# Kernel optimization log

Measured on AMD Instinct MI355X. Metric: run time of the kernel, lower is better.

The kernel has to match this reference:

```python
import jax, jax.numpy as jnp
import numpy as np

D = 512
CELLS = 16
BATCH = 4
SEQ = 1024


def setup_inputs() -> dict:
    key = jax.random.key(0)
    ks = jax.random.split(key, 5)
    x = jax.random.normal(ks[0], (BATCH * CELLS, SEQ, D), dtype=jnp.float32)
    # causal mask: True where attention is disallowed (strict upper triangle)
    m = ~jnp.tril(jnp.ones((SEQ, SEQ), dtype=bool))
    gamma = jnp.ones((D,), dtype=jnp.float32)
    beta = jnp.zeros((D,), dtype=jnp.float32)
    Wg = jax.random.normal(ks[1], (D, D), dtype=jnp.float32) * (D ** -0.5)
    inhibit = jax.random.normal(ks[2], (CELLS, CELLS), dtype=jnp.float32) * 0.02
    phases = jnp.linspace(0.0, 2.0 * np.pi, CELLS, dtype=jnp.float32)
    res_scale = jnp.ones((1,), dtype=jnp.float32) * 0.1
    return {"x": x, "m": m, "gamma": gamma, "beta": beta, "Wg": Wg,
            "inhibit": inhibit, "phases": phases, "res_scale": res_scale,
            "B": BATCH, "T": SEQ}


def _layernorm(x, gamma, beta, eps=1e-5):
    mu = jnp.mean(x, axis=-1, keepdims=True)
    var = jnp.var(x, axis=-1, keepdims=True)
    return (x - mu) * jax.lax.rsqrt(var + eps) * gamma + beta


def reference(x, m, gamma, beta, Wg, inhibit, phases, res_scale, B, T):
    d = x.shape[-1]
    cells = inhibit.shape[0]
    nx = _layernorm(x, gamma, beta)
    qkv = nx @ Wg.T                                  # [BC, T, d]
    att = jnp.einsum('bqd,bkd->bqk', qkv, qkv) * (d ** -0.5)  # [BC, T, T]
    att = jnp.where(m, -jnp.inf, att)
    x = x + jax.nn.softmax(att, axis=-1) @ qkv       # [BC, T, d]
    sync = x.reshape(B, cells, T, d)
    competed = jnp.einsum('bctd,ck->bktd', sync, inhibit)
    pulse = jnp.sin(competed + phases[None, :, None, None])
    return x + pulse.reshape(B * cells, T, d) * res_scale
```

## Files before the change

kernel.cpp:

```cpp
#include <hip/hip_runtime.h>
#include <stdint.h>

#define TSEQ 1024
#define DDIM 512

typedef __attribute__((ext_vector_type(8))) short bf16x8;
typedef __attribute__((ext_vector_type(4))) float f32x4;

#define MFMA(a, b, c) __builtin_amdgcn_mfma_f32_16x16x32_bf16((a), (b), (c), 0, 0, 0)

__device__ __forceinline__ unsigned short f2bf(float f) {
  unsigned int u = __builtin_bit_cast(unsigned int, f);
  u += 0x7FFFu + ((u >> 16) & 1u);
  return (unsigned short)(u >> 16);
}

__device__ __forceinline__ void async_load16(const void* g, void* l) {
  __builtin_amdgcn_global_load_lds(
      (const __attribute__((address_space(1))) unsigned int*)g,
      (__attribute__((address_space(3))) unsigned int*)l, 16, 0, 0);
}

__global__ __launch_bounds__(256) void k_ln(const float* __restrict__ x,
                                            const float* __restrict__ gamma,
                                            const float* __restrict__ beta,
                                            unsigned short* __restrict__ nx) {
  const int wid = threadIdx.x >> 6, lane = threadIdx.x & 63;
  const long long row = (long long)blockIdx.x * 4 + wid;
  const float* xr = x + row * DDIM + lane * 8;
  float4 a = *(const float4*)xr;
  float4 b = *(const float4*)(xr + 4);
  float s = a.x + a.y + a.z + a.w + b.x + b.y + b.z + b.w;
  float s2 = a.x * a.x + a.y * a.y + a.z * a.z + a.w * a.w +
             b.x * b.x + b.y * b.y + b.z * b.z + b.w * b.w;
#pragma unroll
  for (int m = 1; m < 64; m <<= 1) {
    s += __shfl_xor(s, m);
    s2 += __shfl_xor(s2, m);
  }
  const float mu = s * (1.0f / DDIM);
  const float var = s2 * (1.0f / DDIM) - mu * mu;
  const float rsd = rsqrtf(var + 1e-5f);
  const float4 g0 = *(const float4*)(gamma + lane * 8);
  const float4 g1 = *(const float4*)(gamma + lane * 8 + 4);
  const float4 b0 = *(const float4*)(beta + lane * 8);
  const float4 b1 = *(const float4*)(beta + lane * 8 + 4);
  float o0 = (a.x - mu) * rsd * g0.x + b0.x;
  float o1 = (a.y - mu) * rsd * g0.y + b0.y;
  float o2 = (a.z - mu) * rsd * g0.z + b0.z;
  float o3 = (a.w - mu) * rsd * g0.w + b0.w;
  float o4 = (b.x - mu) * rsd * g1.x + b1.x;
  float o5 = (b.y - mu) * rsd * g1.y + b1.y;
  float o6 = (b.z - mu) * rsd * g1.z + b1.z;
  float o7 = (b.w - mu) * rsd * g1.w + b1.w;
  uint4 pk;
  pk.x = f2bf(o0) | ((unsigned)f2bf(o1) << 16);
  pk.y = f2bf(o2) | ((unsigned)f2bf(o3) << 16);
  pk.z = f2bf(o4) | ((unsigned)f2bf(o5) << 16);
  pk.w = f2bf(o6) | ((unsigned)f2bf(o7) << 16);
  *(uint4*)(nx + row * DDIM + lane * 8) = pk;
}

__global__ __launch_bounds__(256) void k_cast(const float* __restrict__ w,
                                              unsigned short* __restrict__ o, int n8) {
  const int i = blockIdx.x * 256 + threadIdx.x;
  if (i >= n8) return;
  const float4 a = *(const float4*)(w + (size_t)i * 8);
  const float4 b = *(const float4*)(w + (size_t)i * 8 + 4);
  uint4 pk;
  pk.x = f2bf(a.x) | ((unsigned)f2bf(a.y) << 16);
  pk.y = f2bf(a.z) | ((unsigned)f2bf(a.w) << 16);
  pk.z = f2bf(b.x) | ((unsigned)f2bf(b.y) << 16);
  pk.w = f2bf(b.z) | ((unsigned)f2bf(b.w) << 16);
  *(uint4*)(o + (size_t)i * 8) = pk;
}

__global__ __launch_bounds__(256, 2) void k_gemm(const unsigned short* __restrict__ A,
                                                 const unsigned short* __restrict__ B,
                                                 unsigned short* __restrict__ C) {
  __shared__ char As[16384];
  __shared__ char Bs[16384];
  const int tid = threadIdx.x;
  const int wid = tid >> 6, lane = tid & 63;
  const int g = lane >> 4, c = lane & 15;
  const int wr = wid >> 1, wc = wid & 1;
  const int bm = blockIdx.y, bn = blockIdx.x;

  int srcoff[4], ldsoff[4];
#pragma unroll
  for (int r = 0; r < 4; ++r) {
    const int aoff = r * 4096 + tid * 16;
    srcoff[r] = (aoff >> 7) * 1024 + (aoff & 127);
    ldsoff[r] = r * 4096 + (wid << 10);
  }
  const char* Ab = (const char*)A + (size_t)bm * 131072;
  const char* Bb = (const char*)B + (size_t)bn * 131072;

  f32x4 acc[4][4] = {};

  for (int ks = 0; ks < 8; ++ks) {
    __syncthreads();
#pragma unroll
    for (int r = 0; r < 4; ++r) {
      async_load16(Ab + ks * 128 + srcoff[r], As + ldsoff[r]);
      async_load16(Bb + ks * 128 + srcoff[r], Bs + ldsoff[r]);
    }
    __syncthreads();
    bf16x8 af[4][2], bfr[4][2];
#pragma unroll
    for (int f = 0; f < 4; ++f) {
#pragma unroll
      for (int kk = 0; kk < 2; ++kk) {
        const int rowa = wr * 64 + f * 16 + c;
        af[f][kk] = *(const bf16x8*)(As + rowa * 128 + (kk * 4 + g) * 16);
        const int rowb = wc * 64 + f * 16 + c;
        bfr[f][kk] = *(const bf16x8*)(Bs + rowb * 128 + (kk * 4 + g) * 16);
      }
    }
#pragma unroll
    for (int i = 0; i < 4; ++i) {
#pragma unroll
      for (int j = 0; j < 4; ++j) {
        acc[i][j] = MFMA(af[i][0], bfr[j][0], acc[i][j]);
        acc[i][j] = MFMA(af[i][1], bfr[j][1], acc[i][j]);
      }
    }
  }
#pragma unroll
  for (int i = 0; i < 4; ++i) {
#pragma unroll
    for (int r = 0; r < 4; ++r) {
      const long long row = (long long)bm * 128 + wr * 64 + i * 16 + g * 4 + r;
#pragma unroll
      for (int j = 0; j < 4; ++j) {
        const int col = bn * 128 + wc * 64 + j * 16 + c;
        C[row * DDIM + col] = f2bf(acc[i][j][r]);
      }
    }
  }
}

__global__ __launch_bounds__(256) void k_vt(const unsigned short* __restrict__ qkv,
                                            unsigned short* __restrict__ qkvT) {
  __shared__ unsigned short t[64][72];
  const int ti = blockIdx.x;
  const int di = blockIdx.y;
  const int bc = blockIdx.z;
  const int tid = threadIdx.x;
  const int r = tid >> 3, c8 = tid & 7;
  const unsigned short* src = qkv + ((size_t)bc * TSEQ + ti * 64) * DDIM + di * 64;
#pragma unroll
  for (int p = 0; p < 2; ++p) {
    const bf16x8 v = *(const bf16x8*)(src + (size_t)(r + p * 32) * DDIM + c8 * 8);
    *(bf16x8*)&t[r + p * 32][c8 * 8] = v;
  }
  __syncthreads();
  unsigned short* dst = qkvT + ((size_t)bc * DDIM + di * 64) * TSEQ + ti * 64;
#pragma unroll
  for (int p = 0; p < 2; ++p) {
    const int d = r + p * 32;
    bf16x8 v;
#pragma unroll
    for (int j = 0; j < 8; ++j) v[j] = t[c8 * 8 + j][d];
    *(bf16x8*)(dst + (size_t)d * TSEQ + c8 * 8) = v;
  }
}

__global__ __launch_bounds__(512, 2) void k_attn(const unsigned short* __restrict__ qkv,
                                                 const unsigned short* __restrict__ qkvT,
                                                 const float* __restrict__ x,
                                                 float* __restrict__ xo) {
  __shared__ char lds[131072];
  const int tid = threadIdx.x;
  const int wid = tid >> 6, lane = tid & 63;
  const int g = lane >> 4, c = lane & 15;
  const int bc = blockIdx.x;
  const size_t bcbase = (size_t)bc * TSEQ * DDIM;
  const float scale = 0.044194173824159216f;

  int e0[2], e1[2];
#pragma unroll
  for (int ft = 0; ft < 2; ++ft) {
    const int row = ((c >> 2) << 3) + (ft << 2) + (c & 3);
    const int kap = ((ft << 2) | (c & 3)) ^ ((c >> 2) << 1);
    e0[ft] = row * 1024 + ((g ^ kap) << 4);
    e1[ft] = row * 1024 + (((4 + g) ^ kap) << 4);
  }

  int soffK[4], soffV[4];
#pragma unroll
  for (int r = 0; r < 4; ++r) {
    const int row = wid * 4 + r;
    const int kap = (row & 7) ^ (((row >> 3) & 3) << 1);
    soffK[r] = row * 1024 + ((lane ^ kap) << 4);
    soffV[r] = (wid * 64 + r * 16 + (lane >> 2)) * 2048 + (lane & 3) * 16;
  }
  const char* kgb = (const char*)(qkv + bcbase);
  const char* vgb = (const char*)qkvT + ((size_t)bc << 20);

#pragma unroll 1
  for (int h = 0; h < 2; ++h) {
    const int qt = h == 0 ? 7 - blockIdx.y : blockIdx.y;
    const int qrow = qt * 128 + wid * 16 + c;
    const int NT = 4 * qt + 4;

    bf16x8 qf[16];
    const unsigned short* qp = qkv + bcbase + (size_t)qrow * DDIM + g * 8;
#pragma unroll
    for (int ks = 0; ks < 16; ++ks) qf[ks] = *(const bf16x8*)(qp + ks * 32);

    f32x4 oacc[32] = {};
    float mrun = -1e30f, lrun = 0.0f;

    {
      char* kb = lds;
      char* vb = lds + 65536;
#pragma unroll
      for (int r = 0; r < 4; ++r) {
        async_load16(kgb + soffK[r], kb + wid * 4096 + r * 1024 + lane * 16);
        async_load16(vgb + soffV[r], vb + wid * 4096 + r * 1024 + lane * 16);
      }
    }

    for (int kvt = 0; kvt < NT; ++kvt) {
      __syncthreads();
      const char* kb = lds + (kvt & 1) * 32768;
      const char* vb = lds + 65536 + (kvt & 1) * 32768;

      if (kvt + 1 < NT) {
        char* kd = lds + ((kvt + 1) & 1) * 32768;
        char* vd = lds + 65536 + ((kvt + 1) & 1) * 32768;
        const char* ksrc = kgb + (kvt + 1) * 32768;
        const char* vsrc = vgb + (kvt + 1) * 64;
#pragma unroll
        for (int r = 0; r < 4; ++r) {
          async_load16(ksrc + soffK[r], kd + wid * 4096 + r * 1024 + lane * 16);
          async_load16(vsrc + soffV[r], vd + wid * 4096 + r * 1024 + lane * 16);
        }
      }

      f32x4 st[2] = {};
      __builtin_amdgcn_s_setprio(1);
#pragma unroll
      for (int ks = 0; ks < 16; ++ks) {
        const int imm = (ks >> 1) * 128;
#pragma unroll
        for (int ft = 0; ft < 2; ++ft) {
          const bf16x8 kf = *(const bf16x8*)(kb + imm + ((ks & 1) ? e1[ft] : e0[ft]));
          st[ft] = MFMA(kf, qf[ks], st[ft]);
        }
      }
      __builtin_amdgcn_s_setprio(0);

      float ex[2][4];
      float mt = -1e30f;
#pragma unroll
      for (int ft = 0; ft < 2; ++ft) {
#pragma unroll
        for (int r = 0; r < 4; ++r) {
          const int kvg = kvt * 32 + g * 8 + ft * 4 + r;
          const float v = st[ft][r] * scale;
          ex[ft][r] = (kvg > qrow) ? -1e30f : v;
          mt = fmaxf(mt, ex[ft][r]);
        }
      }
      mt = fmaxf(mt, __shfl_xor(mt, 16));
      mt = fmaxf(mt, __shfl_xor(mt, 32));
      const float mprev = mrun;
      const float mnew = fmaxf(mprev, mt);
      mrun = mnew;
      float psum = 0.0f;
#pragma unroll
      for (int ft = 0; ft < 2; ++ft) {
#pragma unroll
        for (int r = 0; r < 4; ++r) {
          ex[ft][r] = __expf(ex[ft][r] - mnew);
          psum += ex[ft][r];
        }
      }
      psum += __shfl_xor(psum, 16);
      psum += __shfl_xor(psum, 32);

      if (!__all(mt <= mprev)) {
        const float corr = __expf(mprev - mnew);
        lrun = lrun * corr + psum;
        float cr[4];
#pragma unroll
        for (int r = 0; r < 4; ++r) cr[r] = __shfl(corr, g * 4 + r);
#pragma unroll
        for (int dt = 0; dt < 32; ++dt) {
          oacc[dt][0] *= cr[0];
          oacc[dt][1] *= cr[1];
          oacc[dt][2] *= cr[2];
          oacc[dt][3] *= cr[3];
        }
      } else {
        lrun += psum;
      }

      bf16x8 pa0;
#pragma unroll
      for (int r = 0; r < 4; ++r) {
        pa0[r] = (short)f2bf(ex[0][r]);
        pa0[r + 4] = (short)f2bf(ex[1][r]);
      }

      const char* vp = vb + c * 64 + g * 16;
#pragma unroll
      for (int dt = 0; dt < 32; ++dt) {
        const bf16x8 b0 = *(const bf16x8*)(vp + dt * 1024);
        oacc[dt] = MFMA(pa0, b0, oacc[dt]);
      }
    }

    const float rl = 1.0f / lrun;
    float rlr[4];
#pragma unroll
    for (int r = 0; r < 4; ++r) rlr[r] = __shfl(rl, g * 4 + r);
#pragma unroll
    for (int dt = 0; dt < 32; ++dt) {
#pragma unroll
      for (int r = 0; r < 4; ++r) {
        const size_t off =
            bcbase + (size_t)(qt * 128 + wid * 16 + g * 4 + r) * DDIM + dt * 16 + c;
        xo[off] = x[off] + oacc[dt][r] * rlr[r];
      }
    }
    __syncthreads();
  }
}

__global__ __launch_bounds__(256) void k_mix(float* __restrict__ xo,
                                             const float* __restrict__ inh,
                                             const float* __restrict__ phz,
                                             const float* __restrict__ rsc) {
  __shared__ float sI[256];
  __shared__ float sP[16];
  const int tid = threadIdx.x;
  sI[tid] = inh[tid];
  if (tid < 16) sP[tid] = phz[tid];
  __syncthreads();
  const float rs = rsc[0];
  const int idx = blockIdx.x * 256 + tid;
  const int d4 = idx & 127;
  const int t = (idx >> 7) & 1023;
  const int b = idx >> 17;
  float4* base = (float4*)xo + ((size_t)b * 16 * TSEQ + t) * 128 + d4;
  float4 v[16];
#pragma unroll
  for (int cc = 0; cc < 16; ++cc) v[cc] = base[(size_t)cc * TSEQ * 128];
#pragma unroll
  for (int k = 0; k < 16; ++k) {
    float4 comp = make_float4(0.f, 0.f, 0.f, 0.f);
#pragma unroll
    for (int cc = 0; cc < 16; ++cc) {
      const float w = sI[cc * 16 + k];
      comp.x += v[cc].x * w;
      comp.y += v[cc].y * w;
      comp.z += v[cc].z * w;
      comp.w += v[cc].w * w;
    }
    const float ph = sP[k];
    float4 o;
    o.x = v[k].x + __sinf(comp.x + ph) * rs;
    o.y = v[k].y + __sinf(comp.y + ph) * rs;
    o.z = v[k].z + __sinf(comp.z + ph) * rs;
    o.w = v[k].w + __sinf(comp.w + ph) * rs;
    base[(size_t)k * TSEQ * 128] = o;
  }
}

extern "C" void kernel_launch(void* const* d_in, const int* in_sizes, int n_in,
                              void* d_out, int out_size, void* d_ws, size_t ws_size,
                              hipStream_t stream) {
  const float* x = (const float*)d_in[0];
  const float* gamma = (const float*)d_in[2];
  const float* beta = (const float*)d_in[3];
  const float* Wg = (const float*)d_in[4];
  const float* inh = (const float*)d_in[5];
  const float* phz = (const float*)d_in[6];
  const float* rsc = (const float*)d_in[7];
  float* out = (float*)d_out;

  unsigned short* qkv = (unsigned short*)d_ws;
  unsigned short* qkvT = qkv + (size_t)33554432;
  unsigned short* nx = (unsigned short*)d_out;
  unsigned short* wgb = (unsigned short*)((char*)d_out + 104857600);

  k_cast<<<128, 256, 0, stream>>>(Wg, wgb, 32768);
  k_ln<<<16384, 256, 0, stream>>>(x, gamma, beta, nx);
  k_gemm<<<dim3(4, 512), 256, 0, stream>>>(nx, wgb, qkv);
  k_vt<<<dim3(16, 8, 64), 256, 0, stream>>>(qkv, qkvT);
  k_attn<<<dim3(64, 4), 512, 0, stream>>>(qkv, qkvT, x, out);
  k_mix<<<2048, 256, 0, stream>>>(out, inh, phz, rsc);
}
```

Measured before the change: 350.4 us.

## Fuse V-transpose into GEMM epilogue with MFMA-fragment layout, read V directly

The GEMM epilogue now stages its output tile in LDS and writes a second copy of qkv in a pre-swizzled per-tile layout that matches the MFMA B-fragment order. This removes the separate transpose kernel launch. The attention kernel loads V fragments straight from global memory in that layout instead of async-staging V through LDS, which halves its LDS footprint. In exchange, V reads are no longer double-buffered and now sit on the critical path as global loads, while the GEMM gains extra LDS traffic and a sync.

```diff
diff --git a/kernel.cpp b/kernel.cpp
--- a/kernel.cpp
+++ b/kernel.cpp
@@ -77,9 +77,11 @@
 
 __global__ __launch_bounds__(256, 2) void k_gemm(const unsigned short* __restrict__ A,
                                                  const unsigned short* __restrict__ B,
-                                                 unsigned short* __restrict__ C) {
-  __shared__ char As[16384];
-  __shared__ char Bs[16384];
+                                                 unsigned short* __restrict__ C,
+                                                 unsigned short* __restrict__ W) {
+  __shared__ char sbuf[33280];
+  char* As = sbuf;
+  char* Bs = sbuf + 16384;
   const int tid = threadIdx.x;
   const int wid = tid >> 6, lane = tid & 63;
   const int g = lane >> 4, c = lane & 15;
@@ -126,6 +128,7 @@
       }
     }
   }
+
 #pragma unroll
   for (int i = 0; i < 4; ++i) {
 #pragma unroll
@@ -138,39 +141,38 @@
       }
     }
   }
-}
-
-__global__ __launch_bounds__(256) void k_vt(const unsigned short* __restrict__ qkv,
-                                            unsigned short* __restrict__ qkvT) {
-  __shared__ unsigned short t[64][72];
-  const int ti = blockIdx.x;
-  const int di = blockIdx.y;
-  const int bc = blockIdx.z;
-  const int tid = threadIdx.x;
-  const int r = tid >> 3, c8 = tid & 7;
-  const unsigned short* src = qkv + ((size_t)bc * TSEQ + ti * 64) * DDIM + di * 64;
-#pragma unroll
-  for (int p = 0; p < 2; ++p) {
-    const bf16x8 v = *(const bf16x8*)(src + (size_t)(r + p * 32) * DDIM + c8 * 8);
-    *(bf16x8*)&t[r + p * 32][c8 * 8] = v;
-  }
+
   __syncthreads();
-  unsigned short* dst = qkvT + ((size_t)bc * DDIM + di * 64) * TSEQ + ti * 64;
-#pragma unroll
-  for (int p = 0; p < 2; ++p) {
-    const int d = r + p * 32;
+  unsigned short* tb = (unsigned short*)sbuf;
+#pragma unroll
+  for (int i = 0; i < 4; ++i)
+#pragma unroll
+    for (int j = 0; j < 4; ++j)
+#pragma unroll
+      for (int r = 0; r < 4; ++r)
+        tb[(wr * 64 + i * 16 + g * 4 + r) * 130 + wc * 64 + j * 16 + c] =
+            f2bf(acc[i][j][r]);
+  __syncthreads();
+  const int bc = bm >> 3;
+  const int kvt = (bm & 7) * 4 + wid;
+#pragma unroll
+  for (int dt_l = 0; dt_l < 8; ++dt_l) {
+    const int d_l = dt_l * 16 + c;
+    const int kv0 = wid * 32 + g * 8;
     bf16x8 v;
 #pragma unroll
-    for (int j = 0; j < 8; ++j) v[j] = t[c8 * 8 + j][d];
-    *(bf16x8*)(dst + (size_t)d * TSEQ + c8 * 8) = v;
+    for (int j = 0; j < 8; ++j) v[j] = tb[(kv0 + j) * 130 + d_l];
+    const size_t woff =
+        ((((size_t)bc * 32 + kvt) * 32) + bn * 8 + dt_l) * 1024 + lane * 16;
+    *(bf16x8*)((char*)W + woff) = v;
   }
 }
 
 __global__ __launch_bounds__(512, 2) void k_attn(const unsigned short* __restrict__ qkv,
-                                                 const unsigned short* __restrict__ qkvT,
+                                                 const unsigned short* __restrict__ W,
                                                  const float* __restrict__ x,
                                                  float* __restrict__ xo) {
-  __shared__ char lds[131072];
+  __shared__ char lds[65536];
   const int tid = threadIdx.x;
   const int wid = tid >> 6, lane = tid & 63;
   const int g = lane >> 4, c = lane & 15;
@@ -187,16 +189,15 @@
     e1[ft] = row * 1024 + (((4 + g) ^ kap) << 4);
   }
 
-  int soffK[4], soffV[4];
+  int soffK[4];
 #pragma unroll
   for (int r = 0; r < 4; ++r) {
     const int row = wid * 4 + r;
     const int kap = (row & 7) ^ (((row >> 3) & 3) << 1);
     soffK[r] = row * 1024 + ((lane ^ kap) << 4);
-    soffV[r] = (wid * 64 + r * 16 + (lane >> 2)) * 2048 + (lane & 3) * 16;
   }
   const char* kgb = (const char*)(qkv + bcbase);
-  const char* vgb = (const char*)qkvT + ((size_t)bc << 20);
+  const char* wtb = (const char*)W + ((size_t)bc << 20);
 
 #pragma unroll 1
   for (int h = 0; h < 2; ++h) {
@@ -213,30 +214,21 @@
     float mrun = -1e30f, lrun = 0.0f;
 
     {
-      char* kb = lds;
-      char* vb = lds + 65536;
-#pragma unroll
-      for (int r = 0; r < 4; ++r) {
-        async_load16(kgb + soffK[r], kb + wid * 4096 + r * 1024 + lane * 16);
-        async_load16(vgb + soffV[r], vb + wid * 4096 + r * 1024 + lane * 16);
-      }
+#pragma unroll
+      for (int r = 0; r < 4; ++r)
+        async_load16(kgb + soffK[r], lds + wid * 4096 + r * 1024 + lane * 16);
     }
 
     for (int kvt = 0; kvt < NT; ++kvt) {
       __syncthreads();
       const char* kb = lds + (kvt & 1) * 32768;
-      const char* vb = lds + 65536 + (kvt & 1) * 32768;
 
       if (kvt + 1 < NT) {
         char* kd = lds + ((kvt + 1) & 1) * 32768;
-        char* vd = lds + 65536 + ((kvt + 1) & 1) * 32768;
         const char* ksrc = kgb + (kvt + 1) * 32768;
-        const char* vsrc = vgb + (kvt + 1) * 64;
-#pragma unroll
-        for (int r = 0; r < 4; ++r) {
+#pragma unroll
+        for (int r = 0; r < 4; ++r)
           async_load16(ksrc + soffK[r], kd + wid * 4096 + r * 1024 + lane * 16);
-          async_load16(vsrc + soffV[r], vd + wid * 4096 + r * 1024 + lane * 16);
-        }
       }
 
       f32x4 st[2] = {};
@@ -305,10 +297,10 @@
         pa0[r + 4] = (short)f2bf(ex[1][r]);
       }
 
-      const char* vp = vb + c * 64 + g * 16;
+      const char* wp = wtb + (size_t)kvt * 32768 + lane * 16;
 #pragma unroll
       for (int dt = 0; dt < 32; ++dt) {
-        const bf16x8 b0 = *(const bf16x8*)(vp + dt * 1024);
+        const bf16x8 b0 = *(const bf16x8*)(wp + dt * 1024);
         oacc[dt] = MFMA(pa0, b0, oacc[dt]);
       }
     }
@@ -383,14 +375,13 @@
   float* out = (float*)d_out;
 
   unsigned short* qkv = (unsigned short*)d_ws;
-  unsigned short* qkvT = qkv + (size_t)33554432;
+  unsigned short* W = qkv + (size_t)33554432;
   unsigned short* nx = (unsigned short*)d_out;
   unsigned short* wgb = (unsigned short*)((char*)d_out + 104857600);
 
   k_cast<<<128, 256, 0, stream>>>(Wg, wgb, 32768);
   k_ln<<<16384, 256, 0, stream>>>(x, gamma, beta, nx);
-  k_gemm<<<dim3(4, 512), 256, 0, stream>>>(nx, wgb, qkv);
-  k_vt<<<dim3(16, 8, 64), 256, 0, stream>>>(qkv, qkvT);
-  k_attn<<<dim3(64, 4), 512, 0, stream>>>(qkv, qkvT, x, out);
+  k_gemm<<<dim3(4, 512), 256, 0, stream>>>(nx, wgb, qkv, W);
+  k_attn<<<dim3(64, 4), 512, 0, stream>>>(qkv, W, x, out);
   k_mix<<<2048, 256, 0, stream>>>(out, inh, phz, rsc);
 }
```

Measured after the change: 550.6 us. 1.57x slower.
